# Kernel tuning notes

Measured on AMD Instinct MI355X. Metric: run time of the kernel, lower is better.

The kernel has to match this reference:

```python
import jax, jax.numpy as jnp
import numpy as np

IN_DIM = 512
MEM_DIM = 512
B = 4            # branching factor
LEAVES = 16384   # perfect B-ary tree => N = (B*LEAVES - 1) // (B - 1)


def _build_tree():
    # level sizes from leaves up to root; nodes laid out level-by-level
    sizes = []
    n = LEAVES
    while n >= 1:
        sizes.append(n)
        if n == 1:
            break
        n //= B
    N = sum(sizes)
    children = -np.ones((N, B), dtype=np.int32)
    off_prev, off = 0, sizes[0]
    for l in range(1, len(sizes)):
        nl = sizes[l]
        children[off:off + nl] = off_prev + np.arange(nl * B, dtype=np.int32).reshape(nl, B)
        off_prev, off = off, off + nl
    return N, children


def setup_inputs() -> dict:
    key = jax.random.key(0)
    ks = jax.random.split(key, 9)
    N, children = _build_tree()
    sx = 1.0 / np.sqrt(IN_DIM)
    sh = 1.0 / np.sqrt(MEM_DIM)
    return {
        "x": jax.random.normal(ks[0], (N, IN_DIM), dtype=jnp.float32),
        "children": jnp.asarray(children),
        "W_ioux": jax.random.normal(ks[1], (IN_DIM, 3 * MEM_DIM), dtype=jnp.float32) * sx,
        "b_ioux": jax.random.normal(ks[2], (3 * MEM_DIM,), dtype=jnp.float32) * sx,
        "W_iouh": jax.random.normal(ks[3], (MEM_DIM, 3 * MEM_DIM), dtype=jnp.float32) * sh,
        "b_iouh": jax.random.normal(ks[4], (3 * MEM_DIM,), dtype=jnp.float32) * sh,
        "W_fx": jax.random.normal(ks[5], (IN_DIM, MEM_DIM), dtype=jnp.float32) * sx,
        "b_fx": jax.random.normal(ks[6], (MEM_DIM,), dtype=jnp.float32) * sx,
        "W_fh": jax.random.normal(ks[7], (MEM_DIM, MEM_DIM), dtype=jnp.float32) * sh,
        "b_fh": jax.random.normal(ks[8], (MEM_DIM,), dtype=jnp.float32) * sh,
    }


def _level_sizes(N, Bf):
    sizes = []
    n = (N * (Bf - 1) + 1) // Bf  # leaf count of a perfect Bf-ary tree
    while n >= 1:
        sizes.append(n)
        if n == 1:
            break
        n //= Bf
    return sizes


def reference(x, children, W_ioux, b_ioux, W_iouh, b_iouh, W_fx, b_fx, W_fh, b_fh):
    N, Bf = children.shape
    M = W_iouh.shape[0]
    sizes = _level_sizes(N, Bf)  # static Python ints

    # precompute input-side linears for ALL nodes in two big GEMMs
    x_iou = x @ W_ioux + b_ioux          # [N, 3M]
    x_f = x @ W_fx + b_fx                # [N, M]

    h_all = jnp.zeros((N, M), dtype=x.dtype)
    c_all = jnp.zeros((N, M), dtype=x.dtype)

    off = 0
    for l, nl in enumerate(sizes):
        xi = x_iou[off:off + nl]                        # [nl, 3M]
        xf = x_f[off:off + nl]                          # [nl, M]
        if l == 0:
            # leaves: single zero child (matches torch zeros(1, mem_dim))
            ch_h = jnp.zeros((nl, 1, M), dtype=x.dtype)
            ch_c = jnp.zeros((nl, 1, M), dtype=x.dtype)
        else:
            idx = children[off:off + nl]                # [nl, B]
            ch_h = h_all[idx]                           # [nl, B, M]
            ch_c = c_all[idx]
        h_sum = ch_h.sum(axis=1)                        # [nl, M]
        iou = xi + h_sum @ W_iouh + b_iouh              # [nl, 3M]
        i, o, u = jnp.split(iou, 3, axis=1)
        i = jax.nn.sigmoid(i)
        o = jax.nn.sigmoid(o)
        u = jnp.tanh(u)
        # forget gate per child: sigmoid(fh(h_k) + fx(x))
        f = jax.nn.sigmoid(jnp.einsum('nkm,mp->nkp', ch_h, W_fh) + b_fh + xf[:, None, :])
        c = i * u + (f * ch_c).sum(axis=1)              # [nl, M]
        h = o * jnp.tanh(c)
        h_all = h_all.at[off:off + nl].set(h)
        c_all = c_all.at[off:off + nl].set(c)
        off += nl

    return h_all[N - 1:N]  # root hidden state, [1, M]
```

## Files before the change

### kernel.cpp

```cpp
#include <hip/hip_runtime.h>
#include <cstdint>

using short8 = __attribute__((ext_vector_type(8))) short;
using f32x4  = __attribute__((ext_vector_type(4))) float;
typedef unsigned short ushort_t;

__device__ __forceinline__ ushort_t f2bf(float f) {
    union { float f; unsigned int u; } v; v.f = f;
    unsigned int r = v.u + 0x7FFFu + ((v.u >> 16) & 1u);
    return (ushort_t)(r >> 16);
}
__device__ __forceinline__ float bf2f(ushort_t s) {
    union { unsigned int u; float f; } v; v.u = ((unsigned int)s) << 16;
    return v.f;
}
__device__ __forceinline__ float sigmoidf(float x) { return 1.f / (1.f + expf(-x)); }

__device__ __forceinline__ void async_copy16(void* lds, const void* g) {
    __builtin_amdgcn_global_load_lds((__attribute__((address_space(1))) void*)g,
                                     (__attribute__((address_space(3))) void*)lds,
                                     16, 0, 0);
}

#define KA 1024
#define KB 1536
#define NLEAF 16384
#define NNODE 21845
#define NINT  5461

#define OFF_WTIOUX  0UL
#define OFF_WTIOUH  (OFF_WTIOUX + 1536UL*KB*2)
#define OFF_WTFX    (OFF_WTIOUH + 1536UL*KB*2)
#define OFF_WTFH    (OFF_WTFX   + 512UL*KB*2)
#define OFF_BIASIOU (OFF_WTFH   + 512UL*KB*2)
#define OFF_BIASF   (OFF_BIASIOU + 1536UL*4)
#define OFF_XHL     (OFF_BIASF  + 512UL*4)
#define OFF_HLEAF   (OFF_XHL    + 21848UL*KA*2)
#define OFF_XF      (OFF_HLEAF  + 16384UL*KA*2)
#define OFF_HSUM    (OFF_XF     + 5464UL*512*4)
#define OFF_CLEAF   (OFF_HSUM   + 4096UL*KA*2)
#define OFF_FC      (OFF_CLEAF  + 16384UL*512*4)

__global__ void wsplit_kernel(const float* __restrict__ in, ushort_t* __restrict__ out, int N) {
    __shared__ float t[32][33];
    int kb = blockIdx.x * 32, nb = blockIdx.y * 32;
    for (int i = threadIdx.y; i < 32; i += 8)
        t[i][threadIdx.x] = in[(size_t)(kb + i) * N + nb + threadIdx.x];
    __syncthreads();
    for (int i = threadIdx.y; i < 32; i += 8) {
        float v = t[threadIdx.x][i];
        ushort_t hi = f2bf(v);
        ushort_t lo = f2bf(v - bf2f(hi));
        size_t row = (size_t)(nb + i) * KB + kb + threadIdx.x;
        out[row]        = hi;
        out[row + 512]  = hi;
        out[row + 1024] = lo;
    }
}

__global__ void bias_kernel(const float* __restrict__ b_ioux, const float* __restrict__ b_iouh,
                            const float* __restrict__ b_fx, const float* __restrict__ b_fh,
                            float* __restrict__ bias_iou, float* __restrict__ bias_f) {
    int t = blockIdx.x * blockDim.x + threadIdx.x;
    if (t < 1536) bias_iou[t] = b_ioux[t] + b_iouh[t];
    if (t < 512)  bias_f[t]   = b_fx[t] + b_fh[t];
}

__global__ void xexp_kernel(const float* __restrict__ x, ushort_t* __restrict__ xe, int n4) {
    int t = blockIdx.x * blockDim.x + threadIdx.x;
    if (t >= n4) return;
    int j = t >> 7, m4 = (t & 127) * 4;
    float4 v = *(const float4*)&x[(size_t)j * 512 + m4];
    ushort4 hi, lo;
    hi.x = f2bf(v.x); lo.x = f2bf(v.x - bf2f(hi.x));
    hi.y = f2bf(v.y); lo.y = f2bf(v.y - bf2f(hi.y));
    hi.z = f2bf(v.z); lo.z = f2bf(v.z - bf2f(hi.z));
    hi.w = f2bf(v.w); lo.w = f2bf(v.w - bf2f(hi.w));
    ushort_t* row = xe + (size_t)j * KA;
    *(ushort4*)&row[m4] = hi;
    *(ushort4*)&row[512 + m4] = lo;
}

__global__ void hsum_kernel(const ushort_t* __restrict__ h_hl, ushort_t* __restrict__ hsum_hl,
                            int n4) {
    int t = blockIdx.x * blockDim.x + threadIdx.x;
    if (t >= n4) return;
    int j = t >> 7, m4 = (t & 127) * 4;
    const ushort_t* base = h_hl + (size_t)(4 * j) * KA;
    float s0 = 0.f, s1 = 0.f, s2 = 0.f, s3 = 0.f;
#pragma unroll
    for (int r = 0; r < 4; ++r) {
        ushort4 h4 = *(const ushort4*)&base[(size_t)r * KA + m4];
        ushort4 l4 = *(const ushort4*)&base[(size_t)r * KA + 512 + m4];
        s0 += bf2f(h4.x) + bf2f(l4.x);
        s1 += bf2f(h4.y) + bf2f(l4.y);
        s2 += bf2f(h4.z) + bf2f(l4.z);
        s3 += bf2f(h4.w) + bf2f(l4.w);
    }
    ushort4 hi, lo;
    hi.x = f2bf(s0); lo.x = f2bf(s0 - bf2f(hi.x));
    hi.y = f2bf(s1); lo.y = f2bf(s1 - bf2f(hi.y));
    hi.z = f2bf(s2); lo.z = f2bf(s2 - bf2f(hi.z));
    hi.w = f2bf(s3); lo.w = f2bf(s3 - bf2f(hi.w));
    ushort_t* row = hsum_hl + (size_t)j * KA;
    *(ushort4*)&row[m4] = hi;
    *(ushort4*)&row[512 + m4] = lo;
}

__global__ __launch_bounds__(256)
void gemm_kernel(int M,
                 const ushort_t* __restrict__ a1,
                 const ushort_t* __restrict__ b1,
                 float* __restrict__ outf, int ldout) {
    __shared__ __align__(16) ushort_t Al[128 * 32];
    __shared__ __align__(16) ushort_t Bl[128 * 32];

    const int tid  = threadIdx.x;
    const int lane = tid & 63, wv = tid >> 6;
    const int l15  = lane & 15, quad = lane >> 4;
    const int wm   = wv >> 1, wn = wv & 1;
    const int m0   = blockIdx.x * 128;
    const int n0   = blockIdx.y * 128;

    const int srow = wv * 16 + (lane >> 2);
    const int kch  = ((lane & 3) ^ ((lane >> 3) & 3)) * 8;
    const int swz  = (quad ^ ((l15 >> 1) & 3)) * 8;

    const ushort_t* a1p[2]; const ushort_t* b1p[2];
#pragma unroll
    for (int r = 0; r < 2; ++r) {
        int rl = m0 + srow + r * 64; if (rl > M - 1) rl = M - 1;
        a1p[r] = a1 + (size_t)rl * KA + kch;
        int nb = n0 + srow + r * 64;
        b1p[r] = b1 + (size_t)nb * KB + kch;
    }

    f32x4 acc[4][4] = {};
    for (int k0 = 0; k0 < KB; k0 += 32) {
        int ka = (k0 < KA) ? k0 : k0 - KA;
        __syncthreads();
#pragma unroll
        for (int r = 0; r < 2; ++r) {
            async_copy16(&Al[(size_t)(wv * 16 + r * 64) * 32], a1p[r] + ka);
            async_copy16(&Bl[(size_t)(wv * 16 + r * 64) * 32], b1p[r] + k0);
        }
        __syncthreads();

        short8 aF[4], bF[4];
#pragma unroll
        for (int i = 0; i < 4; ++i) {
            aF[i] = *(const short8*)&Al[(size_t)(wm * 64 + i * 16 + l15) * 32 + swz];
            bF[i] = *(const short8*)&Bl[(size_t)(wn * 64 + i * 16 + l15) * 32 + swz];
        }
#pragma unroll
        for (int i = 0; i < 4; ++i)
#pragma unroll
            for (int j = 0; j < 4; ++j)
                acc[i][j] = __builtin_amdgcn_mfma_f32_16x16x32_bf16(aF[i], bF[j], acc[i][j], 0, 0, 0);
    }

#pragma unroll
    for (int i = 0; i < 4; ++i) {
        int mbase = m0 + wm * 64 + i * 16 + quad * 4;
#pragma unroll
        for (int j = 0; j < 4; ++j) {
            int n = n0 + wn * 64 + j * 16 + l15;
#pragma unroll
            for (int r = 0; r < 4; ++r) {
                int m = mbase + r;
                if (m < M) outf[(size_t)m * ldout + n] = acc[i][j][r];
            }
        }
    }
}

__global__ __launch_bounds__(256)
void combined_kernel(int nl,
                     const ushort_t* __restrict__ child_h, const float* __restrict__ c_prev,
                     const float* __restrict__ xf, const float* __restrict__ bias_f,
                     float* __restrict__ fc_out,
                     const ushort_t* __restrict__ x_lvl, const ushort_t* __restrict__ hsum,
                     const ushort_t* __restrict__ Wfh,
                     const ushort_t* __restrict__ Wioux, const ushort_t* __restrict__ Wiouh,
                     float* __restrict__ iou_f, ushort_t* __restrict__ iou_b) {
    __shared__ __align__(16) ushort_t Al[128 * 32];
    __shared__ __align__(16) ushort_t Bl[128 * 32];

    const int by = blockIdx.y;
    const bool fpath = by < 4;
    const int M = fpath ? 4 * nl : nl;
    const int m0 = blockIdx.x * 128;
    if (m0 >= M) return;
    const int n0 = (fpath ? by : by - 4) * 128;

    const ushort_t* A1 = fpath ? child_h : x_lvl;
    const ushort_t* A2 = fpath ? nullptr : hsum;
    const ushort_t* B1 = fpath ? Wfh : Wioux;
    const ushort_t* B2 = fpath ? nullptr : Wiouh;

    const int tid  = threadIdx.x;
    const int lane = tid & 63, wv = tid >> 6;
    const int l15  = lane & 15, quad = lane >> 4;
    const int wm   = wv >> 1, wn = wv & 1;

    const int srow = wv * 16 + (lane >> 2);
    const int kch  = ((lane & 3) ^ ((lane >> 3) & 3)) * 8;
    const int swz  = (quad ^ ((l15 >> 1) & 3)) * 8;

    const ushort_t* a1p[2]; const ushort_t* a2p[2];
    const ushort_t* b1p[2]; const ushort_t* b2p[2];
#pragma unroll
    for (int r = 0; r < 2; ++r) {
        int rl = m0 + srow + r * 64; if (rl > M - 1) rl = M - 1;
        a1p[r] = A1 + (size_t)rl * KA + kch;
        a2p[r] = A2 ? A2 + (size_t)rl * KA + kch : nullptr;
        int nb = n0 + srow + r * 64;
        b1p[r] = B1 + (size_t)nb * KB + kch;
        b2p[r] = B2 ? B2 + (size_t)nb * KB + kch : nullptr;
    }

    f32x4 acc[4][4] = {};
    const int nphase = A2 ? 2 : 1;
    for (int ph = 0; ph < nphase; ++ph) {
        for (int k0 = 0; k0 < KB; k0 += 32) {
            int ka = (k0 < KA) ? k0 : k0 - KA;
            __syncthreads();
#pragma unroll
            for (int r = 0; r < 2; ++r) {
                async_copy16(&Al[(size_t)(wv * 16 + r * 64) * 32], (ph ? a2p[r] : a1p[r]) + ka);
                async_copy16(&Bl[(size_t)(wv * 16 + r * 64) * 32], (ph ? b2p[r] : b1p[r]) + k0);
            }
            __syncthreads();

            short8 aF[4], bF[4];
#pragma unroll
            for (int i = 0; i < 4; ++i) {
                aF[i] = *(const short8*)&Al[(size_t)(wm * 64 + i * 16 + l15) * 32 + swz];
                bF[i] = *(const short8*)&Bl[(size_t)(wn * 64 + i * 16 + l15) * 32 + swz];
            }
#pragma unroll
            for (int i = 0; i < 4; ++i)
#pragma unroll
                for (int j = 0; j < 4; ++j)
                    acc[i][j] = __builtin_amdgcn_mfma_f32_16x16x32_bf16(aF[i], bF[j], acc[i][j], 0, 0, 0);
        }
    }

    if (fpath) {
#pragma unroll
        for (int i = 0; i < 4; ++i) {
            int mbase = m0 + wm * 64 + i * 16 + quad * 4;
            if (mbase < M) {
                int jg = mbase >> 2;
#pragma unroll
                for (int j = 0; j < 4; ++j) {
                    int n = n0 + wn * 64 + j * 16 + l15;
                    float add = xf[(size_t)jg * 512 + n] + bias_f[n];
                    float fc = 0.f;
#pragma unroll
                    for (int r = 0; r < 4; ++r) {
                        float f = sigmoidf(acc[i][j][r] + add);
                        fc += f * c_prev[(size_t)(mbase + r) * 512 + n];
                    }
                    fc_out[(size_t)jg * 512 + n] = fc;
                }
            }
        }
    } else {
#pragma unroll
        for (int i = 0; i < 4; ++i) {
            int mbase = m0 + wm * 64 + i * 16 + quad * 4;
#pragma unroll
            for (int j = 0; j < 4; ++j) {
                int n = n0 + wn * 64 + j * 16 + l15;
#pragma unroll
                for (int r = 0; r < 4; ++r) {
                    int m = mbase + r;
                    if (m < M) {
                        if (iou_b) iou_b[(size_t)m * 1536 + n] = f2bf(acc[i][j][r]);
                        else       iou_f[(size_t)m * 1536 + n] = acc[i][j][r];
                    }
                }
            }
        }
    }
}

__global__ __launch_bounds__(256)
void fused_leaf_kernel(int M,
                       const ushort_t* __restrict__ a1,
                       const ushort_t* __restrict__ b1,
                       const float* __restrict__ bias_iou,
                       float* __restrict__ c_out,
                       ushort_t* __restrict__ h_out) {
    __shared__ __align__(16) ushort_t Al[128 * 32];
    __shared__ __align__(16) ushort_t Bl[3 * 64 * 32];

    const int tid  = threadIdx.x;
    const int lane = tid & 63, wv = tid >> 6;
    const int l15  = lane & 15, quad = lane >> 4;
    const int m0   = blockIdx.x * 128;
    const int n0   = blockIdx.y * 64;

    const int srow = wv * 16 + (lane >> 2);
    const int kch  = ((lane & 3) ^ ((lane >> 3) & 3)) * 8;
    const int swz  = (quad ^ ((l15 >> 1) & 3)) * 8;

    const ushort_t* a1p[2]; const ushort_t* b1p[3];
#pragma unroll
    for (int r = 0; r < 2; ++r) {
        int rl = m0 + srow + r * 64; if (rl > M - 1) rl = M - 1;
        a1p[r] = a1 + (size_t)rl * KA + kch;
    }
#pragma unroll
    for (int g = 0; g < 3; ++g)
        b1p[g] = b1 + (size_t)(g * 512 + n0 + srow) * KB + kch;

    f32x4 acc[3][2][4] = {};
    for (int k0 = 0; k0 < KB; k0 += 32) {
        int ka = (k0 < KA) ? k0 : k0 - KA;
        __syncthreads();
#pragma unroll
        for (int r = 0; r < 2; ++r)
            async_copy16(&Al[(size_t)(wv * 16 + r * 64) * 32], a1p[r] + ka);
#pragma unroll
        for (int g = 0; g < 3; ++g)
            async_copy16(&Bl[(size_t)(g * 64 + wv * 16) * 32], b1p[g] + k0);
        __syncthreads();

        short8 aF[2];
#pragma unroll
        for (int i = 0; i < 2; ++i)
            aF[i] = *(const short8*)&Al[(size_t)(wv * 32 + i * 16 + l15) * 32 + swz];
#pragma unroll
        for (int g = 0; g < 3; ++g) {
            short8 bF[4];
#pragma unroll
            for (int j = 0; j < 4; ++j)
                bF[j] = *(const short8*)&Bl[(size_t)(g * 64 + j * 16 + l15) * 32 + swz];
#pragma unroll
            for (int i = 0; i < 2; ++i)
#pragma unroll
                for (int j = 0; j < 4; ++j)
                    acc[g][i][j] = __builtin_amdgcn_mfma_f32_16x16x32_bf16(aF[i], bF[j], acc[g][i][j], 0, 0, 0);
        }
    }

#pragma unroll
    for (int i = 0; i < 2; ++i) {
        int mbase = m0 + wv * 32 + i * 16 + quad * 4;
#pragma unroll
        for (int r = 0; r < 4; ++r) {
            int m = mbase + r;
            if (m < M) {
#pragma unroll
                for (int j = 0; j < 4; ++j) {
                    int n = n0 + j * 16 + l15;
                    float iv = sigmoidf(acc[0][i][j][r] + bias_iou[n]);
                    float ov = sigmoidf(acc[1][i][j][r] + bias_iou[512 + n]);
                    float uv = tanhf(  acc[2][i][j][r] + bias_iou[1024 + n]);
                    float c = iv * uv;
                    float h = ov * tanhf(c);
                    c_out[(size_t)m * 512 + n] = c;
                    ushort_t hi = f2bf(h), lo = f2bf(h - bf2f(hi));
                    h_out[(size_t)m * KA + n] = hi;
                    h_out[(size_t)m * KA + 512 + n] = lo;
                }
            }
        }
    }
}

template <bool IOU_BF>
__global__ void cell_kernel(const void* __restrict__ iou_v, const float* __restrict__ bias_iou,
                            const float* __restrict__ fc,
                            ushort_t* __restrict__ h_out, float* __restrict__ c_out,
                            int n4, float* __restrict__ outp) {
    int t = blockIdx.x * blockDim.x + threadIdx.x;
    if (t >= n4) return;
    int j = t >> 7, m4 = (t & 127) * 4;
    float pi[4], po[4], pu[4];
    if constexpr (IOU_BF) {
        const ushort_t* row = (const ushort_t*)iou_v + (size_t)j * 1536;
        ushort4 a = *(const ushort4*)&row[m4];
        ushort4 b = *(const ushort4*)&row[512 + m4];
        ushort4 c = *(const ushort4*)&row[1024 + m4];
        pi[0]=bf2f(a.x); pi[1]=bf2f(a.y); pi[2]=bf2f(a.z); pi[3]=bf2f(a.w);
        po[0]=bf2f(b.x); po[1]=bf2f(b.y); po[2]=bf2f(b.z); po[3]=bf2f(b.w);
        pu[0]=bf2f(c.x); pu[1]=bf2f(c.y); pu[2]=bf2f(c.z); pu[3]=bf2f(c.w);
    } else {
        const float* row = (const float*)iou_v + (size_t)j * 1536;
        float4 a = *(const float4*)&row[m4];
        float4 b = *(const float4*)&row[512 + m4];
        float4 c = *(const float4*)&row[1024 + m4];
        pi[0]=a.x; pi[1]=a.y; pi[2]=a.z; pi[3]=a.w;
        po[0]=b.x; po[1]=b.y; po[2]=b.z; po[3]=b.w;
        pu[0]=c.x; pu[1]=c.y; pu[2]=c.z; pu[3]=c.w;
    }
    float4 bi = *(const float4*)&bias_iou[m4];
    float4 bo = *(const float4*)&bias_iou[512 + m4];
    float4 bu = *(const float4*)&bias_iou[1024 + m4];
    float4 fcv = *(const float4*)&fc[(size_t)j * 512 + m4];
    float bia[4] = {bi.x, bi.y, bi.z, bi.w};
    float boa[4] = {bo.x, bo.y, bo.z, bo.w};
    float bua[4] = {bu.x, bu.y, bu.z, bu.w};
    float fca[4] = {fcv.x, fcv.y, fcv.z, fcv.w};
    float cv[4], hv[4];
#pragma unroll
    for (int q = 0; q < 4; ++q) {
        float iv = sigmoidf(pi[q] + bia[q]);
        float ov = sigmoidf(po[q] + boa[q]);
        float uv = tanhf(  pu[q] + bua[q]);
        cv[q] = iv * uv + fca[q];
        hv[q] = ov * tanhf(cv[q]);
    }
    *(float4*)&c_out[(size_t)j * 512 + m4] = float4{cv[0], cv[1], cv[2], cv[3]};
    ushort4 hi, lo;
    hi.x = f2bf(hv[0]); lo.x = f2bf(hv[0] - bf2f(hi.x));
    hi.y = f2bf(hv[1]); lo.y = f2bf(hv[1] - bf2f(hi.y));
    hi.z = f2bf(hv[2]); lo.z = f2bf(hv[2] - bf2f(hi.z));
    hi.w = f2bf(hv[3]); lo.w = f2bf(hv[3] - bf2f(hi.w));
    ushort_t* hr = h_out + (size_t)j * KA;
    *(ushort4*)&hr[m4] = hi;
    *(ushort4*)&hr[512 + m4] = lo;
    if (outp) *(float4*)&outp[m4] = float4{hv[0], hv[1], hv[2], hv[3]};
}

extern "C" void kernel_launch(void* const* d_in, const int* in_sizes, int n_in,
                              void* d_out, int out_size, void* d_ws, size_t ws_size,
                              hipStream_t stream) {
    const float* x       = (const float*)d_in[0];
    const float* W_ioux  = (const float*)d_in[2];
    const float* b_ioux  = (const float*)d_in[3];
    const float* W_iouh  = (const float*)d_in[4];
    const float* b_iouh  = (const float*)d_in[5];
    const float* W_fx    = (const float*)d_in[6];
    const float* b_fx    = (const float*)d_in[7];
    const float* W_fh    = (const float*)d_in[8];
    const float* b_fh    = (const float*)d_in[9];
    float* out = (float*)d_out;
    char* ws = (char*)d_ws;

    ushort_t* WTioux = (ushort_t*)(ws + OFF_WTIOUX);
    ushort_t* WTiouh = (ushort_t*)(ws + OFF_WTIOUH);
    ushort_t* WTfx   = (ushort_t*)(ws + OFF_WTFX);
    ushort_t* WTfh   = (ushort_t*)(ws + OFF_WTFH);
    float*    bias_iou = (float*)(ws + OFF_BIASIOU);
    float*    bias_f   = (float*)(ws + OFF_BIASF);
    ushort_t* x_hl   = (ushort_t*)(ws + OFF_XHL);
    ushort_t* h_int  = x_hl;
    ushort_t* iou_b  = x_hl + (size_t)5464 * KA;
    float*    iou_f  = (float*)iou_b;
    ushort_t* h_leaf = (ushort_t*)(ws + OFF_HLEAF);
    float*    c_int  = (float*)(ws + OFF_HLEAF);
    float*    xf32   = (float*)(ws + OFF_XF);
    ushort_t* hsum_hl= (ushort_t*)(ws + OFF_HSUM);
    float*    c_leaf = (float*)(ws + OFF_CLEAF);
    float*    fc_buf = (float*)(ws + OFF_FC);

    wsplit_kernel<<<dim3(16, 48), dim3(32, 8), 0, stream>>>(W_ioux, WTioux, 1536);
    wsplit_kernel<<<dim3(16, 48), dim3(32, 8), 0, stream>>>(W_iouh, WTiouh, 1536);
    wsplit_kernel<<<dim3(16, 16), dim3(32, 8), 0, stream>>>(W_fx,   WTfx,   512);
    wsplit_kernel<<<dim3(16, 16), dim3(32, 8), 0, stream>>>(W_fh,   WTfh,   512);
    bias_kernel<<<6, 256, 0, stream>>>(b_ioux, b_iouh, b_fx, b_fh, bias_iou, bias_f);

    xexp_kernel<<<(NNODE * 128 + 255) / 256, 256, 0, stream>>>(x, x_hl, NNODE * 128);

    gemm_kernel<<<dim3(43, 4), 256, 0, stream>>>(
        NINT, x_hl + (size_t)NLEAF * KA, WTfx, xf32, 512);

    fused_leaf_kernel<<<dim3(128, 8), 256, 0, stream>>>(
        NLEAF, x_hl, WTioux, bias_iou, c_leaf, h_leaf);

    const int sizes[8] = {16384, 4096, 1024, 256, 64, 16, 4, 1};
    int off = 0;
    for (int l = 1; l < 8; ++l) {
        int off_prev = off;
        off += sizes[l - 1];
        int ioff = off - NLEAF;
        int nl = sizes[l];
        int M4 = 4 * nl;
        int n4 = nl * 128;

        const ushort_t* child_h = (l == 1) ? h_leaf : h_int + (size_t)(off_prev - NLEAF) * KA;
        const float*    child_c = (l == 1) ? c_leaf : c_int + (size_t)(off_prev - NLEAF) * 512;

        hsum_kernel<<<(n4 + 255) / 256, 256, 0, stream>>>(child_h, hsum_hl, n4);

        bool use_bf = (l == 1);
        combined_kernel<<<dim3((M4 + 127) / 128, 16), 256, 0, stream>>>(
            nl, child_h, child_c, xf32 + (size_t)ioff * 512, bias_f, fc_buf,
            x_hl + (size_t)off * KA, hsum_hl, WTfh, WTioux, WTiouh,
            use_bf ? nullptr : iou_f, use_bf ? iou_b : nullptr);

        if (use_bf)
            cell_kernel<true><<<(n4 + 255) / 256, 256, 0, stream>>>(
                iou_b, bias_iou, fc_buf, h_int + (size_t)ioff * KA,
                c_int + (size_t)ioff * 512, n4, nullptr);
        else
            cell_kernel<false><<<(n4 + 255) / 256, 256, 0, stream>>>(
                iou_f, bias_iou, fc_buf, h_int + (size_t)ioff * KA,
                c_int + (size_t)ioff * 512, n4, (l == 7) ? out : nullptr);
    }
    (void)d_in; (void)in_sizes; (void)n_in; (void)out_size; (void)ws_size;
}
```

Baseline: 728.3 us.

## Fuse small upper tree levels into one persistent kernel with grid barriers

Replaces the per-level launch sequence (hsum, combined GEMM, cell) for the five smallest tree levels with a single persistent 256-block kernel that runs each level as fp32 CUDA-core GEMV-style work, separated by atomic grid barriers. Small levels use a split-K scheme with partial buffers and a separate reduction/cell phase. This removes many kernel launches and tail-latency stalls on tiny levels. The cost is spin barriers that depend on all 256 blocks being co-resident, plus an extra fp32 h output from the level-2 cell kernel.

```diff
diff --git a/kernel.cpp b/kernel.cpp
--- a/kernel.cpp
+++ b/kernel.cpp
@@ -60,10 +60,12 @@
 
 __global__ void bias_kernel(const float* __restrict__ b_ioux, const float* __restrict__ b_iouh,
                             const float* __restrict__ b_fx, const float* __restrict__ b_fh,
-                            float* __restrict__ bias_iou, float* __restrict__ bias_f) {
+                            float* __restrict__ bias_iou, float* __restrict__ bias_f,
+                            unsigned* __restrict__ bar) {
     int t = blockIdx.x * blockDim.x + threadIdx.x;
     if (t < 1536) bias_iou[t] = b_ioux[t] + b_iouh[t];
     if (t < 512)  bias_f[t]   = b_fx[t] + b_fh[t];
+    if (blockIdx.x == 0 && threadIdx.x == 0) { bar[0] = 0u; bar[1] = 0u; }
 }
 
 __global__ void xexp_kernel(const float* __restrict__ x, ushort_t* __restrict__ xe, int n4) {
@@ -375,7 +377,7 @@
 __global__ void cell_kernel(const void* __restrict__ iou_v, const float* __restrict__ bias_iou,
                             const float* __restrict__ fc,
                             ushort_t* __restrict__ h_out, float* __restrict__ c_out,
-                            int n4, float* __restrict__ outp) {
+                            int n4, float* __restrict__ outp, float* __restrict__ hf_out) {
     int t = blockIdx.x * blockDim.x + threadIdx.x;
     if (t >= n4) return;
     int j = t >> 7, m4 = (t & 127) * 4;
@@ -423,7 +425,179 @@
     ushort_t* hr = h_out + (size_t)j * KA;
     *(ushort4*)&hr[m4] = hi;
     *(ushort4*)&hr[512 + m4] = lo;
+    if (hf_out) *(float4*)&hf_out[(size_t)j * 512 + m4] = float4{hv[0], hv[1], hv[2], hv[3]};
     if (outp) *(float4*)&outp[m4] = float4{hv[0], hv[1], hv[2], hv[3]};
+}
+
+
+__device__ __forceinline__ void grid_barrier(unsigned* bar, unsigned base, unsigned step) {
+    __syncthreads();
+    if (threadIdx.x == 0) {
+        __threadfence();
+        unsigned old = __hip_atomic_fetch_add(&bar[0], 1u, __ATOMIC_ACQ_REL, __HIP_MEMORY_SCOPE_AGENT);
+        if (((old + 1u) & 255u) == 0u)
+            __hip_atomic_fetch_add(&bar[1], 1u, __ATOMIC_ACQ_REL, __HIP_MEMORY_SCOPE_AGENT);
+        while ((unsigned)(__hip_atomic_load(&bar[1], __ATOMIC_ACQUIRE, __HIP_MEMORY_SCOPE_AGENT) - base) < step)
+            __builtin_amdgcn_s_sleep(2);
+        __threadfence();
+    }
+    __syncthreads();
+}
+
+template <int S>
+__device__ void tail_gemm(int nl, int ioff, int ioffp,
+                          const float* __restrict__ x, float* __restrict__ hf,
+                          float* __restrict__ c_int, const float* __restrict__ xf,
+                          const float* __restrict__ Wx, const float* __restrict__ Wh,
+                          const float* __restrict__ Wf,
+                          const float* __restrict__ bias_iou, const float* __restrict__ bias_f,
+                          float* __restrict__ iou_part, float* __restrict__ f_part, int tid) {
+    const int JG = (nl + 3) >> 2;
+    const int unitsG = JG * 512 * S;
+    for (int u = tid; u < unitsG; u += 65536) {
+        const int n = u & 511;
+        int t2 = u >> 9;
+        int s, jg;
+        if constexpr (S == 1) { s = 0; jg = t2; }
+        else                  { s = t2 & (S - 1); jg = t2 / S; }
+        jg = __builtin_amdgcn_readfirstlane(jg);
+        s  = __builtin_amdgcn_readfirstlane(s);
+        const int jbase = jg << 2;
+
+        const float* xr[4]; const float* hb[4];
+#pragma unroll
+        for (int p = 0; p < 4; ++p) {
+            int jc = jbase + p; if (jc > nl - 1) jc = nl - 1;
+            xr[p] = x + (size_t)(ioff + 16384 + jc) * 512;
+            hb[p] = hf + (size_t)(ioffp - 4096 + 4 * jc) * 512;
+        }
+        float aI[4][3] = {}; float aF[4][4] = {};
+#pragma unroll 4
+        for (int k = s; k < 512; k += S) {
+            const size_t kr = (size_t)k * 1536;
+            float w0 = Wx[kr + n], w1 = Wx[kr + 512 + n], w2 = Wx[kr + 1024 + n];
+#pragma unroll
+            for (int p = 0; p < 4; ++p) {
+                float xa = xr[p][k];
+                aI[p][0] += xa * w0; aI[p][1] += xa * w1; aI[p][2] += xa * w2;
+            }
+        }
+#pragma unroll 4
+        for (int k = s; k < 512; k += S) {
+            const size_t kr = (size_t)k * 1536;
+            float w0 = Wh[kr + n], w1 = Wh[kr + 512 + n], w2 = Wh[kr + 1024 + n];
+            float wf = Wf[(size_t)k * 512 + n];
+#pragma unroll
+            for (int p = 0; p < 4; ++p) {
+                float h0 = hb[p][k], h1 = hb[p][512 + k], h2 = hb[p][1024 + k], h3 = hb[p][1536 + k];
+                float hs = (h0 + h1) + (h2 + h3);
+                aI[p][0] += hs * w0; aI[p][1] += hs * w1; aI[p][2] += hs * w2;
+                aF[p][0] += h0 * wf; aF[p][1] += h1 * wf; aF[p][2] += h2 * wf; aF[p][3] += h3 * wf;
+            }
+        }
+        if constexpr (S == 1) {
+#pragma unroll
+            for (int p = 0; p < 4; ++p) {
+                int j = jbase + p;
+                if (j < nl) {
+                    float iv = sigmoidf(aI[p][0] + bias_iou[n]);
+                    float ov = sigmoidf(aI[p][1] + bias_iou[512 + n]);
+                    float uv = tanhf(  aI[p][2] + bias_iou[1024 + n]);
+                    float add = xf[(size_t)(ioff + j) * 512 + n] + bias_f[n];
+                    float fc = 0.f;
+#pragma unroll
+                    for (int r = 0; r < 4; ++r)
+                        fc += sigmoidf(aF[p][r] + add) * c_int[(size_t)(ioffp + 4 * j + r) * 512 + n];
+                    float c = iv * uv + fc;
+                    float h = ov * tanhf(c);
+                    c_int[(size_t)(ioff + j) * 512 + n] = c;
+                    hf[(size_t)(ioff - 4096 + j) * 512 + n] = h;
+                }
+            }
+        } else {
+#pragma unroll
+            for (int p = 0; p < 4; ++p) {
+                int j = jbase + p;
+                if (j < nl) {
+#pragma unroll
+                    for (int g = 0; g < 3; ++g)
+                        iou_part[(((size_t)s * nl + j) * 3 + g) * 512 + n] = aI[p][g];
+#pragma unroll
+                    for (int r = 0; r < 4; ++r)
+                        f_part[((size_t)s * 4 * nl + 4 * j + r) * 512 + n] = aF[p][r];
+                }
+            }
+        }
+    }
+}
+
+template <int S>
+__device__ void tail_cell(int nl, int ioff, int ioffp,
+                          float* __restrict__ hf, float* __restrict__ c_int,
+                          const float* __restrict__ xf,
+                          const float* __restrict__ bias_iou, const float* __restrict__ bias_f,
+                          const float* __restrict__ iou_part, const float* __restrict__ f_part,
+                          float* __restrict__ out, int tid) {
+    const int unitsC = nl * 512;
+    for (int u = tid; u < unitsC; u += 65536) {
+        const int n = u & 511;
+        const int j = u >> 9;
+        float g0 = bias_iou[n], g1 = bias_iou[512 + n], g2 = bias_iou[1024 + n];
+        float f0 = 0.f, f1 = 0.f, f2 = 0.f, f3 = 0.f;
+#pragma unroll 4
+        for (int s = 0; s < S; ++s) {
+            const float* ip = iou_part + (((size_t)s * nl + j) * 3) * 512 + n;
+            g0 += ip[0]; g1 += ip[512]; g2 += ip[1024];
+            const float* fp = f_part + ((size_t)s * 4 * nl + 4 * j) * 512 + n;
+            f0 += fp[0]; f1 += fp[512]; f2 += fp[1024]; f3 += fp[1536];
+        }
+        float iv = sigmoidf(g0), ov = sigmoidf(g1), uv = tanhf(g2);
+        float add = xf[(size_t)(ioff + j) * 512 + n] + bias_f[n];
+        float fc = sigmoidf(f0 + add) * c_int[(size_t)(ioffp + 4 * j + 0) * 512 + n]
+                 + sigmoidf(f1 + add) * c_int[(size_t)(ioffp + 4 * j + 1) * 512 + n]
+                 + sigmoidf(f2 + add) * c_int[(size_t)(ioffp + 4 * j + 2) * 512 + n]
+                 + sigmoidf(f3 + add) * c_int[(size_t)(ioffp + 4 * j + 3) * 512 + n];
+        float c = iv * uv + fc;
+        float h = ov * tanhf(c);
+        c_int[(size_t)(ioff + j) * 512 + n] = c;
+        hf[(size_t)(ioff - 4096 + j) * 512 + n] = h;
+        if (ioff == 5460) out[n] = h;
+    }
+}
+
+__global__ __launch_bounds__(256, 4)
+void tail_kernel(const float* __restrict__ x, float* __restrict__ hf,
+                 float* __restrict__ c_int, const float* __restrict__ xf,
+                 const float* __restrict__ Wx, const float* __restrict__ Wh,
+                 const float* __restrict__ Wf,
+                 const float* __restrict__ bias_iou, const float* __restrict__ bias_f,
+                 float* __restrict__ iou_part, float* __restrict__ f_part,
+                 unsigned* __restrict__ bar, float* __restrict__ out) {
+    const int tid = blockIdx.x * 256 + threadIdx.x;
+    __shared__ unsigned s_base;
+    if (threadIdx.x == 0)
+        s_base = __hip_atomic_load(&bar[1], __ATOMIC_RELAXED, __HIP_MEMORY_SCOPE_AGENT);
+    __syncthreads();
+    const unsigned base = s_base;
+    unsigned step = 0;
+
+    tail_gemm<1>(256, 5120, 4096, x, hf, c_int, xf, Wx, Wh, Wf, bias_iou, bias_f, iou_part, f_part, tid);
+    grid_barrier(bar, base, ++step);
+    tail_gemm<4>(64, 5376, 5120, x, hf, c_int, xf, Wx, Wh, Wf, bias_iou, bias_f, iou_part, f_part, tid);
+    grid_barrier(bar, base, ++step);
+    tail_cell<4>(64, 5376, 5120, hf, c_int, xf, bias_iou, bias_f, iou_part, f_part, out, tid);
+    grid_barrier(bar, base, ++step);
+    tail_gemm<16>(16, 5440, 5376, x, hf, c_int, xf, Wx, Wh, Wf, bias_iou, bias_f, iou_part, f_part, tid);
+    grid_barrier(bar, base, ++step);
+    tail_cell<16>(16, 5440, 5376, hf, c_int, xf, bias_iou, bias_f, iou_part, f_part, out, tid);
+    grid_barrier(bar, base, ++step);
+    tail_gemm<32>(4, 5456, 5440, x, hf, c_int, xf, Wx, Wh, Wf, bias_iou, bias_f, iou_part, f_part, tid);
+    grid_barrier(bar, base, ++step);
+    tail_cell<32>(4, 5456, 5440, hf, c_int, xf, bias_iou, bias_f, iou_part, f_part, out, tid);
+    grid_barrier(bar, base, ++step);
+    tail_gemm<32>(1, 5460, 5456, x, hf, c_int, xf, Wx, Wh, Wf, bias_iou, bias_f, iou_part, f_part, tid);
+    grid_barrier(bar, base, ++step);
+    tail_cell<32>(1, 5460, 5456, hf, c_int, xf, bias_iou, bias_f, iou_part, f_part, out, tid);
 }
 
 extern "C" void kernel_launch(void* const* d_in, const int* in_sizes, int n_in,
@@ -457,12 +631,16 @@
     ushort_t* hsum_hl= (ushort_t*)(ws + OFF_HSUM);
     float*    c_leaf = (float*)(ws + OFF_CLEAF);
     float*    fc_buf = (float*)(ws + OFF_FC);
+    float*    hf32     = (float*)(ws + OFF_CLEAF);
+    float*    iou_part = iou_f;
+    float*    f_part   = iou_f + 393216;
+    unsigned* barp     = (unsigned*)(x_hl + (size_t)21845 * KA);
 
     wsplit_kernel<<<dim3(16, 48), dim3(32, 8), 0, stream>>>(W_ioux, WTioux, 1536);
     wsplit_kernel<<<dim3(16, 48), dim3(32, 8), 0, stream>>>(W_iouh, WTiouh, 1536);
     wsplit_kernel<<<dim3(16, 16), dim3(32, 8), 0, stream>>>(W_fx,   WTfx,   512);
     wsplit_kernel<<<dim3(16, 16), dim3(32, 8), 0, stream>>>(W_fh,   WTfh,   512);
-    bias_kernel<<<6, 256, 0, stream>>>(b_ioux, b_iouh, b_fx, b_fh, bias_iou, bias_f);
+    bias_kernel<<<6, 256, 0, stream>>>(b_ioux, b_iouh, b_fx, b_fh, bias_iou, bias_f, barp);
 
     xexp_kernel<<<(NNODE * 128 + 255) / 256, 256, 0, stream>>>(x, x_hl, NNODE * 128);
 
@@ -472,35 +650,30 @@
     fused_leaf_kernel<<<dim3(128, 8), 256, 0, stream>>>(
         NLEAF, x_hl, WTioux, bias_iou, c_leaf, h_leaf);
 
-    const int sizes[8] = {16384, 4096, 1024, 256, 64, 16, 4, 1};
-    int off = 0;
-    for (int l = 1; l < 8; ++l) {
-        int off_prev = off;
-        off += sizes[l - 1];
-        int ioff = off - NLEAF;
-        int nl = sizes[l];
-        int M4 = 4 * nl;
-        int n4 = nl * 128;
-
-        const ushort_t* child_h = (l == 1) ? h_leaf : h_int + (size_t)(off_prev - NLEAF) * KA;
-        const float*    child_c = (l == 1) ? c_leaf : c_int + (size_t)(off_prev - NLEAF) * 512;
-
-        hsum_kernel<<<(n4 + 255) / 256, 256, 0, stream>>>(child_h, hsum_hl, n4);
-
-        bool use_bf = (l == 1);
+    {
+        const int nl = 4096, n4 = nl * 128, M4 = 4 * nl;
+        hsum_kernel<<<(n4 + 255) / 256, 256, 0, stream>>>(h_leaf, hsum_hl, n4);
         combined_kernel<<<dim3((M4 + 127) / 128, 16), 256, 0, stream>>>(
-            nl, child_h, child_c, xf32 + (size_t)ioff * 512, bias_f, fc_buf,
-            x_hl + (size_t)off * KA, hsum_hl, WTfh, WTioux, WTiouh,
-            use_bf ? nullptr : iou_f, use_bf ? iou_b : nullptr);
-
-        if (use_bf)
-            cell_kernel<true><<<(n4 + 255) / 256, 256, 0, stream>>>(
-                iou_b, bias_iou, fc_buf, h_int + (size_t)ioff * KA,
-                c_int + (size_t)ioff * 512, n4, nullptr);
-        else
-            cell_kernel<false><<<(n4 + 255) / 256, 256, 0, stream>>>(
-                iou_f, bias_iou, fc_buf, h_int + (size_t)ioff * KA,
-                c_int + (size_t)ioff * 512, n4, (l == 7) ? out : nullptr);
-    }
+            nl, h_leaf, c_leaf, xf32, bias_f, fc_buf,
+            x_hl + (size_t)16384 * KA, hsum_hl, WTfh, WTioux, WTiouh,
+            nullptr, iou_b);
+        cell_kernel<true><<<(n4 + 255) / 256, 256, 0, stream>>>(
+            iou_b, bias_iou, fc_buf, h_int, c_int, n4, nullptr, nullptr);
+    }
+    {
+        const int nl = 1024, n4 = nl * 128, M4 = 4 * nl, ioff = 4096;
+        hsum_kernel<<<(n4 + 255) / 256, 256, 0, stream>>>(h_int, hsum_hl, n4);
+        combined_kernel<<<dim3((M4 + 127) / 128, 16), 256, 0, stream>>>(
+            nl, h_int, c_int, xf32 + (size_t)ioff * 512, bias_f, fc_buf,
+            x_hl + (size_t)20480 * KA, hsum_hl, WTfh, WTioux, WTiouh,
+            iou_f, nullptr);
+        cell_kernel<false><<<(n4 + 255) / 256, 256, 0, stream>>>(
+            iou_f, bias_iou, fc_buf, h_int + (size_t)ioff * KA, c_int + (size_t)ioff * 512,
+            n4, nullptr, hf32);
+    }
+    tail_kernel<<<256, 256, 0, stream>>>(
+        x, hf32, c_int, xf32, W_ioux, W_iouh, W_fh, bias_iou, bias_f,
+        iou_part, f_part, barp, out);
+
     (void)d_in; (void)in_sizes; (void)n_in; (void)out_size; (void)ws_size;
 }
```

New measurement: 1.908 ms. 2.62x slower.
